# Kernel optimization log

Hardware: AMD Instinct MI355X
Metric: run time of the kernel (lower is better)

Reference implementation:

```python
import jax, jax.numpy as jnp
import numpy as np

N = 16384
C = 128
F = 128

def setup_inputs() -> dict:
    key = jax.random.key(0)
    k1, k2, k3, k4 = jax.random.split(key, 4)
    X = jax.random.normal(k1, (N, C), dtype=jnp.float32)
    adj = jax.random.uniform(k2, (N, N), dtype=jnp.float32)
    W = jax.random.normal(k3, (C, F), dtype=jnp.float32) * 0.05
    b = jax.random.normal(k4, (F,), dtype=jnp.float32) * 0.05
    return {"X": X, "adj": adj, "W": W, "b": b}

def reference(X, adj, W, b):
    # adj_hat = adj + I (self-loops)
    adj_hat = adj + jnp.eye(adj.shape[0], dtype=adj.dtype)
    # D^{-1/2}: inverse of sqrt of the diagonal degree matrix == 1/sqrt(rowsum)
    d_inv_sqrt = 1.0 / jnp.sqrt(jnp.sum(adj_hat, axis=1))  # [N]
    # Symmetric normalization via row/col scaling (same math as D^-1/2 @ A @ D^-1/2)
    adj_norm = adj_hat * d_inv_sqrt[:, None] * d_inv_sqrt[None, :]
    # Feature transform first (N*C*F) then aggregate (N*N*F)
    out = adj_norm @ (X @ W) + b
    return jax.nn.relu(out)
```

## Files before the change

kernel.cpp:

```cpp
#include <hip/hip_runtime.h>
#include <hip/hip_bf16.h>

typedef __attribute__((ext_vector_type(8))) short short8;
typedef __attribute__((ext_vector_type(4))) float f32x4;

#define N_NODES 16384
#define FEAT 128
#define NTILES 256
#define KSPLIT 2
#define NT2 (NTILES / KSPLIT)

__device__ __forceinline__ short f2bf(float x) {
  union { float f; unsigned u; } v;
  v.f = x;
  unsigned r = v.u + 0x7fffu + ((v.u >> 16) & 1u);
  return (short)(r >> 16);
}

__global__ __launch_bounds__(256) void rowsum_kernel(
    const float* __restrict__ adj, float* __restrict__ dinv)
{
  const int row = blockIdx.x;
  const float4* p4 = (const float4*)(adj + (size_t)row * N_NODES);
  float s = 0.f;
  #pragma unroll 4
  for (int i = threadIdx.x; i < N_NODES / 4; i += 256) {
    float4 v = p4[i];
    s += (v.x + v.y) + (v.z + v.w);
  }
  #pragma unroll
  for (int off = 32; off > 0; off >>= 1) s += __shfl_down(s, off, 64);
  __shared__ float part[4];
  if ((threadIdx.x & 63) == 0) part[threadIdx.x >> 6] = s;
  __syncthreads();
  if (threadIdx.x == 0) {
    float tot = (part[0] + part[1]) + (part[2] + part[3]) + 1.0f;
    dinv[row] = rsqrtf(tot);
  }
}

__global__ __launch_bounds__(256) void xw_kernel(
    const float* __restrict__ X, const float* __restrict__ W,
    const float* __restrict__ dinv,
    __hip_bfloat16* __restrict__ Ypack)
{
  __shared__ __align__(16) float Ws[64][128];
  __shared__ __align__(16) float Xs[32][128];
  __shared__ __align__(16) short Ts[128][40];
  const int tid = threadIdx.x;
  const int row0 = blockIdx.x << 5;

  {
    const float4* Xg = (const float4*)(X + ((size_t)row0 << 7));
    float4* Xl = (float4*)&Xs[0][0];
    #pragma unroll
    for (int i = 0; i < 4; ++i) Xl[tid + (i << 8)] = Xg[tid + (i << 8)];
  }
  const int f  = tid & 127;
  const int rr = tid >> 7;
  float acc[16];
  #pragma unroll
  for (int k = 0; k < 16; ++k) acc[k] = 0.f;

  for (int cc = 0; cc < 2; ++cc) {
    __syncthreads();
    {
      const float4* Wg = (const float4*)(W + ((size_t)cc << 13));
      float4* Wl = (float4*)&Ws[0][0];
      #pragma unroll
      for (int i = 0; i < 8; ++i) Wl[tid + (i << 8)] = Wg[tid + (i << 8)];
    }
    __syncthreads();
    for (int c4 = 0; c4 < 16; ++c4) {
      const int cl = c4 << 2;
      const float w0 = Ws[cl + 0][f];
      const float w1 = Ws[cl + 1][f];
      const float w2 = Ws[cl + 2][f];
      const float w3 = Ws[cl + 3][f];
      const int cg = (cc << 6) + cl;
      #pragma unroll
      for (int k = 0; k < 16; ++k) {
        const float4 x = *(const float4*)&Xs[rr + (k << 1)][cg];
        acc[k] += x.x * w0 + x.y * w1 + x.z * w2 + x.w * w3;
      }
    }
  }
  #pragma unroll
  for (int k = 0; k < 16; ++k) {
    const int r = rr + (k << 1);
    const float dv = dinv[row0 + r];
    Ts[f][r] = f2bf(acc[k] * dv);
  }
  __syncthreads();
  {
    const int f2 = tid >> 1;
    const int h  = (tid & 1) << 4;
    const short8 v0 = *(const short8*)&Ts[f2][h];
    const short8 v1 = *(const short8*)&Ts[f2][h + 8];
    short* o = (short*)Ypack;
    *(short8*)(o + (size_t)(row0 + h) * FEAT + (f2 << 3))     = v0;
    *(short8*)(o + (size_t)(row0 + h + 8) * FEAT + (f2 << 3)) = v1;
  }
}

__global__ __launch_bounds__(512, 4) void spmm_kernel(
    const float* __restrict__ A,
    const __hip_bfloat16* __restrict__ Ypack,
    float* __restrict__ pws)
{
  __shared__ __align__(16) short As[2][4096];
  __shared__ __align__(16) short Bs[2][8192];

  const int tid = threadIdx.x;
  const int bid = blockIdx.x;
  const int mt  = bid & 255;
  const int s   = bid >> 8;
  const int row0 = mt << 6;

  const int ar  = tid >> 3;
  const int akg = tid & 7;
  const float* Ag = A + (size_t)(row0 + ar) * N_NODES + (s * NT2 << 6) + (akg << 3);
  const short* Yg = (const short*)Ypack + ((size_t)(s * NT2) << 13) + (tid << 4);

  const int wid  = tid >> 6;
  const int wm   = wid >> 1;
  const int wf   = wid & 1;
  const int lane = tid & 63;
  const int lm   = lane & 15;
  const int lkg  = (lane >> 4);
  const int myrow = (wm << 4) + lm;

  f32x4 acc[4];
  #pragma unroll
  for (int c = 0; c < 4; ++c) acc[c] = (f32x4){0.f, 0.f, 0.f, 0.f};

  float4 a0A, a1A, a0B, a1B;
  short8 y0A, y1A, y0B, y1B;

#define LOADT(T, A0_, A1_, Y0_, Y1_)                                           \
  {                                                                            \
    const float* ap = Ag + ((size_t)(T) << 6);                                 \
    A0_ = *(const float4*)(ap);                                                \
    A1_ = *(const float4*)(ap + 4);                                            \
    const short* yp = Yg + ((size_t)(T) << 13);                                \
    Y0_ = *(const short8*)(yp);                                                \
    Y1_ = *(const short8*)(yp + 8);                                            \
  }

#define STORET(T, P, A0_, A1_, Y0_, Y1_)                                       \
  {                                                                            \
    if (s * NT2 + (T) == mt && (ar >> 3) == akg) {          \
      const int j = ar & 7;                                                    \
      A0_.x += (j == 0) ? 1.f : 0.f;  A0_.y += (j == 1) ? 1.f : 0.f;           \
      A0_.z += (j == 2) ? 1.f : 0.f;  A0_.w += (j == 3) ? 1.f : 0.f;           \
      A1_.x += (j == 4) ? 1.f : 0.f;  A1_.y += (j == 5) ? 1.f : 0.f;           \
      A1_.z += (j == 6) ? 1.f : 0.f;  A1_.w += (j == 7) ? 1.f : 0.f;           \
    }                                                                          \
    short8 av;                                                                 \
    av[0] = f2bf(A0_.x); av[1] = f2bf(A0_.y); av[2] = f2bf(A0_.z);             \
    av[3] = f2bf(A0_.w); av[4] = f2bf(A1_.x); av[5] = f2bf(A1_.y);             \
    av[6] = f2bf(A1_.z); av[7] = f2bf(A1_.w);                                  \
    *(short8*)&As[P][(akg << 9) + (ar << 3)] = av;                             \
    *(short8*)&Bs[P][tid << 4]       = Y0_;                                    \
    *(short8*)&Bs[P][(tid << 4) + 8] = Y1_;                                    \
  }

#define COMP(P)                                                                \
  {                                                                            \
    const short8 af0 = *(const short8*)&As[P][(lkg << 9) + (myrow << 3)];      \
    acc[0] = __builtin_amdgcn_mfma_f32_16x16x32_bf16(af0,                      \
        *(const short8*)&Bs[P][(lkg << 10) + (((wf << 6) + lm) << 3)], acc[0], 0, 0, 0); \
    acc[1] = __builtin_amdgcn_mfma_f32_16x16x32_bf16(af0,                      \
        *(const short8*)&Bs[P][(lkg << 10) + (((wf << 6) + 16 + lm) << 3)], acc[1], 0, 0, 0); \
    acc[2] = __builtin_amdgcn_mfma_f32_16x16x32_bf16(af0,                      \
        *(const short8*)&Bs[P][(lkg << 10) + (((wf << 6) + 32 + lm) << 3)], acc[2], 0, 0, 0); \
    acc[3] = __builtin_amdgcn_mfma_f32_16x16x32_bf16(af0,                      \
        *(const short8*)&Bs[P][(lkg << 10) + (((wf << 6) + 48 + lm) << 3)], acc[3], 0, 0, 0); \
    const short8 af1 = *(const short8*)&As[P][((4 + lkg) << 9) + (myrow << 3)];\
    acc[0] = __builtin_amdgcn_mfma_f32_16x16x32_bf16(af1,                      \
        *(const short8*)&Bs[P][((4 + lkg) << 10) + (((wf << 6) + lm) << 3)], acc[0], 0, 0, 0); \
    acc[1] = __builtin_amdgcn_mfma_f32_16x16x32_bf16(af1,                      \
        *(const short8*)&Bs[P][((4 + lkg) << 10) + (((wf << 6) + 16 + lm) << 3)], acc[1], 0, 0, 0); \
    acc[2] = __builtin_amdgcn_mfma_f32_16x16x32_bf16(af1,                      \
        *(const short8*)&Bs[P][((4 + lkg) << 10) + (((wf << 6) + 32 + lm) << 3)], acc[2], 0, 0, 0); \
    acc[3] = __builtin_amdgcn_mfma_f32_16x16x32_bf16(af1,                      \
        *(const short8*)&Bs[P][((4 + lkg) << 10) + (((wf << 6) + 48 + lm) << 3)], acc[3], 0, 0, 0); \
  }

#define BAR()                                                                  \
  asm volatile("s_waitcnt lgkmcnt(0)" ::: "memory");                           \
  __builtin_amdgcn_s_barrier();

  LOADT(0, a0A, a1A, y0A, y1A)
  LOADT(1, a0B, a1B, y0B, y1B)
  STORET(0, 0, a0A, a1A, y0A, y1A)
  BAR()

  for (int t = 0; t < NT2; t += 2) {
    if (t + 2 < NT2) LOADT(t + 2, a0A, a1A, y0A, y1A)
    __builtin_amdgcn_s_setprio(1);
    COMP(0)
    __builtin_amdgcn_s_setprio(0);
    if (t + 1 < NT2) STORET(t + 1, 1, a0B, a1B, y0B, y1B)
    BAR()
    if (t + 3 < NT2) LOADT(t + 3, a0B, a1B, y0B, y1B)
    __builtin_amdgcn_s_setprio(1);
    COMP(1)
    __builtin_amdgcn_s_setprio(0);
    if (t + 2 < NT2) STORET(t + 2, 0, a0A, a1A, y0A, y1A)
    BAR()
  }

  float* pp = pws + ((size_t)(s * N_NODES + row0)) * FEAT;
  const int lr = (lane >> 4) << 2;
  #pragma unroll
  for (int c = 0; c < 4; ++c) {
    const int col = (wf << 6) + (c << 4) + lm;
    #pragma unroll
    for (int r = 0; r < 4; ++r) {
      pp[(size_t)((wm << 4) + lr + r) * FEAT + col] = acc[c][r];
    }
  }
#undef LOADT
#undef STORET
#undef COMP
#undef BAR
}

__global__ __launch_bounds__(256) void reduce_kernel(
    const float* __restrict__ pws, const float* __restrict__ dinv,
    const float* __restrict__ bias, float* __restrict__ out)
{
  const int idx4 = blockIdx.x * 256 + threadIdx.x;
  const int row  = idx4 >> 5;
  const int f4   = idx4 & 31;
  const float4 p0 = ((const float4*)pws)[idx4];
  const float4 p1 = ((const float4*)pws)[idx4 + (N_NODES * FEAT / 4)];
  const float4 bv = ((const float4*)bias)[f4];
  const float  d  = dinv[row];
  float4 v;
  v.x = d * (p0.x + p1.x) + bv.x;
  v.y = d * (p0.y + p1.y) + bv.y;
  v.z = d * (p0.z + p1.z) + bv.z;
  v.w = d * (p0.w + p1.w) + bv.w;
  v.x = v.x > 0.f ? v.x : 0.f;
  v.y = v.y > 0.f ? v.y : 0.f;
  v.z = v.z > 0.f ? v.z : 0.f;
  v.w = v.w > 0.f ? v.w : 0.f;
  ((float4*)out)[idx4] = v;
}

extern "C" void kernel_launch(void* const* d_in, const int* in_sizes, int n_in,
                              void* d_out, int out_size, void* d_ws, size_t ws_size,
                              hipStream_t stream) {
  const float* X   = (const float*)d_in[0];
  const float* adj = (const float*)d_in[1];
  const float* W   = (const float*)d_in[2];
  const float* b   = (const float*)d_in[3];
  float* out = (float*)d_out;

  float* dinv           = (float*)d_ws;
  __hip_bfloat16* Ypack = (__hip_bfloat16*)((char*)d_ws + (1 << 16));
  float* pws            = (float*)((char*)d_ws + (1 << 16) + (1 << 22));

  rowsum_kernel<<<N_NODES, 256, 0, stream>>>(adj, dinv);
  xw_kernel<<<N_NODES / 32, 256, 0, stream>>>(X, W, dinv, Ypack);
  spmm_kernel<<<NTILES * KSPLIT, 512, 0, stream>>>(adj, Ypack, pws);
  reduce_kernel<<<N_NODES * FEAT / 4 / 256, 256, 0, stream>>>(pws, dinv, b, out);
}
```

Baseline: 409.2 us.

## Load Y tiles directly into LDS with triple buffering and remap block order

```diff
diff --git a/kernel.cpp b/kernel.cpp
--- a/kernel.cpp
+++ b/kernel.cpp
@@ -109,25 +109,26 @@
     float* __restrict__ pws)
 {
   __shared__ __align__(16) short As[2][4096];
-  __shared__ __align__(16) short Bs[2][8192];
+  __shared__ __align__(16) short Bs[3][8192];
 
   const int tid = threadIdx.x;
-  const int bid = blockIdx.x;
-  const int mt  = bid & 255;
-  const int s   = bid >> 8;
+  const int rb  = blockIdx.x;
+  const int lb  = ((rb & 7) << 6) | (rb >> 3);
+  const int mt  = lb & 255;
+  const int s   = lb >> 8;
   const int row0 = mt << 6;
 
   const int ar  = tid >> 3;
   const int akg = tid & 7;
   const float* Ag = A + (size_t)(row0 + ar) * N_NODES + (s * NT2 << 6) + (akg << 3);
-  const short* Yg = (const short*)Ypack + ((size_t)(s * NT2) << 13) + (tid << 4);
+  const short* Yg = (const short*)Ypack + ((size_t)(s * NT2) << 13) + (tid << 3);
 
   const int wid  = tid >> 6;
   const int wm   = wid >> 1;
   const int wf   = wid & 1;
   const int lane = tid & 63;
   const int lm   = lane & 15;
-  const int lkg  = (lane >> 4);
+  const int lkg  = lane >> 4;
   const int myrow = (wm << 4) + lm;
 
   f32x4 acc[4];
@@ -135,19 +136,27 @@
   for (int c = 0; c < 4; ++c) acc[c] = (f32x4){0.f, 0.f, 0.f, 0.f};
 
   float4 a0A, a1A, a0B, a1B;
-  short8 y0A, y1A, y0B, y1B;
-
-#define LOADT(T, A0_, A1_, Y0_, Y1_)                                           \
+
+#define GLDSY(T, P)                                                            \
+  {                                                                            \
+    const short* ys_ = Yg + ((size_t)(T) << 13);                               \
+    __builtin_amdgcn_global_load_lds(                                          \
+        (const __attribute__((address_space(1))) void*)ys_,                    \
+        (__attribute__((address_space(3))) void*)&Bs[P][wid << 9], 16, 0, 0);  \
+    __builtin_amdgcn_global_load_lds(                                          \
+        (const __attribute__((address_space(1))) void*)(ys_ + 4096),           \
+        (__attribute__((address_space(3))) void*)&Bs[P][4096 + (wid << 9)],    \
+        16, 0, 0);                                                             \
+  }
+
+#define LOADA(T, A0_, A1_)                                                     \
   {                                                                            \
     const float* ap = Ag + ((size_t)(T) << 6);                                 \
     A0_ = *(const float4*)(ap);                                                \
     A1_ = *(const float4*)(ap + 4);                                            \
-    const short* yp = Yg + ((size_t)(T) << 13);                                \
-    Y0_ = *(const short8*)(yp);                                                \
-    Y1_ = *(const short8*)(yp + 8);                                            \
-  }
-
-#define STORET(T, P, A0_, A1_, Y0_, Y1_)                                       \
+  }
+
+#define STORA(T, P, A0_, A1_)                                                  \
   {                                                                            \
     if (s * NT2 + (T) == mt && (ar >> 3) == akg) {          \
       const int j = ar & 7;                                                    \
@@ -161,54 +170,62 @@
     av[3] = f2bf(A0_.w); av[4] = f2bf(A1_.x); av[5] = f2bf(A1_.y);             \
     av[6] = f2bf(A1_.z); av[7] = f2bf(A1_.w);                                  \
     *(short8*)&As[P][(akg << 9) + (ar << 3)] = av;                             \
-    *(short8*)&Bs[P][tid << 4]       = Y0_;                                    \
-    *(short8*)&Bs[P][(tid << 4) + 8] = Y1_;                                    \
-  }
-
-#define COMP(P)                                                                \
-  {                                                                            \
-    const short8 af0 = *(const short8*)&As[P][(lkg << 9) + (myrow << 3)];      \
+  }
+
+#define COMP(AP, BP)                                                           \
+  {                                                                            \
+    const short8 af0 = *(const short8*)&As[AP][(lkg << 9) + (myrow << 3)];     \
     acc[0] = __builtin_amdgcn_mfma_f32_16x16x32_bf16(af0,                      \
-        *(const short8*)&Bs[P][(lkg << 10) + (((wf << 6) + lm) << 3)], acc[0], 0, 0, 0); \
+        *(const short8*)&Bs[BP][(lkg << 10) + (((wf << 6) + lm) << 3)], acc[0], 0, 0, 0); \
     acc[1] = __builtin_amdgcn_mfma_f32_16x16x32_bf16(af0,                      \
-        *(const short8*)&Bs[P][(lkg << 10) + (((wf << 6) + 16 + lm) << 3)], acc[1], 0, 0, 0); \
+        *(const short8*)&Bs[BP][(lkg << 10) + (((wf << 6) + 16 + lm) << 3)], acc[1], 0, 0, 0); \
     acc[2] = __builtin_amdgcn_mfma_f32_16x16x32_bf16(af0,                      \
-        *(const short8*)&Bs[P][(lkg << 10) + (((wf << 6) + 32 + lm) << 3)], acc[2], 0, 0, 0); \
+        *(const short8*)&Bs[BP][(lkg << 10) + (((wf << 6) + 32 + lm) << 3)], acc[2], 0, 0, 0); \
     acc[3] = __builtin_amdgcn_mfma_f32_16x16x32_bf16(af0,                      \
-        *(const short8*)&Bs[P][(lkg << 10) + (((wf << 6) + 48 + lm) << 3)], acc[3], 0, 0, 0); \
-    const short8 af1 = *(const short8*)&As[P][((4 + lkg) << 9) + (myrow << 3)];\
+        *(const short8*)&Bs[BP][(lkg << 10) + (((wf << 6) + 48 + lm) << 3)], acc[3], 0, 0, 0); \
+    const short8 af1 = *(const short8*)&As[AP][((4 + lkg) << 9) + (myrow << 3)]; \
     acc[0] = __builtin_amdgcn_mfma_f32_16x16x32_bf16(af1,                      \
-        *(const short8*)&Bs[P][((4 + lkg) << 10) + (((wf << 6) + lm) << 3)], acc[0], 0, 0, 0); \
+        *(const short8*)&Bs[BP][((4 + lkg) << 10) + (((wf << 6) + lm) << 3)], acc[0], 0, 0, 0); \
     acc[1] = __builtin_amdgcn_mfma_f32_16x16x32_bf16(af1,                      \
-        *(const short8*)&Bs[P][((4 + lkg) << 10) + (((wf << 6) + 16 + lm) << 3)], acc[1], 0, 0, 0); \
+        *(const short8*)&Bs[BP][((4 + lkg) << 10) + (((wf << 6) + 16 + lm) << 3)], acc[1], 0, 0, 0); \
     acc[2] = __builtin_amdgcn_mfma_f32_16x16x32_bf16(af1,                      \
-        *(const short8*)&Bs[P][((4 + lkg) << 10) + (((wf << 6) + 32 + lm) << 3)], acc[2], 0, 0, 0); \
+        *(const short8*)&Bs[BP][((4 + lkg) << 10) + (((wf << 6) + 32 + lm) << 3)], acc[2], 0, 0, 0); \
     acc[3] = __builtin_amdgcn_mfma_f32_16x16x32_bf16(af1,                      \
-        *(const short8*)&Bs[P][((4 + lkg) << 10) + (((wf << 6) + 48 + lm) << 3)], acc[3], 0, 0, 0); \
-  }
-
-#define BAR()                                                                  \
-  asm volatile("s_waitcnt lgkmcnt(0)" ::: "memory");                           \
+        *(const short8*)&Bs[BP][((4 + lkg) << 10) + (((wf << 6) + 48 + lm) << 3)], acc[3], 0, 0, 0); \
+  }
+
+  GLDSY(0, 0)
+  LOADA(0, a0A, a1A)
+  GLDSY(1, 1)
+  LOADA(1, a0B, a1B)
+  STORA(0, 0, a0A, a1A)
+  asm volatile("s_waitcnt lgkmcnt(0)" ::: "memory");
   __builtin_amdgcn_s_barrier();
 
-  LOADT(0, a0A, a1A, y0A, y1A)
-  LOADT(1, a0B, a1B, y0B, y1B)
-  STORET(0, 0, a0A, a1A, y0A, y1A)
-  BAR()
-
+  int bp = 0;
   for (int t = 0; t < NT2; t += 2) {
-    if (t + 2 < NT2) LOADT(t + 2, a0A, a1A, y0A, y1A)
+    int bw = bp + 2; if (bw >= 3) bw -= 3;
+    if (t + 2 < NT2) { GLDSY(t + 2, bw) LOADA(t + 2, a0A, a1A) }
     __builtin_amdgcn_s_setprio(1);
-    COMP(0)
+    COMP(0, bp)
     __builtin_amdgcn_s_setprio(0);
-    if (t + 1 < NT2) STORET(t + 1, 1, a0B, a1B, y0B, y1B)
-    BAR()
-    if (t + 3 < NT2) LOADT(t + 3, a0B, a1B, y0B, y1B)
+    if (t + 1 < NT2) STORA(t + 1, 1, a0B, a1B)
+    if (t + 2 < NT2) { asm volatile("s_waitcnt vmcnt(4)" ::: "memory"); }
+    else             { asm volatile("s_waitcnt vmcnt(0)" ::: "memory"); }
+    asm volatile("s_waitcnt lgkmcnt(0)" ::: "memory");
+    __builtin_amdgcn_s_barrier();
+    int bp1 = bp + 1; if (bp1 >= 3) bp1 -= 3;
+    int bw1 = bp1 + 2; if (bw1 >= 3) bw1 -= 3;
+    if (t + 3 < NT2) { GLDSY(t + 3, bw1) LOADA(t + 3, a0B, a1B) }
     __builtin_amdgcn_s_setprio(1);
-    COMP(1)
+    COMP(1, bp1)
     __builtin_amdgcn_s_setprio(0);
-    if (t + 2 < NT2) STORET(t + 2, 0, a0A, a1A, y0A, y1A)
-    BAR()
+    if (t + 2 < NT2) STORA(t + 2, 0, a0A, a1A)
+    if (t + 3 < NT2) { asm volatile("s_waitcnt vmcnt(4)" ::: "memory"); }
+    else             { asm volatile("s_waitcnt vmcnt(0)" ::: "memory"); }
+    asm volatile("s_waitcnt lgkmcnt(0)" ::: "memory");
+    __builtin_amdgcn_s_barrier();
+    bp = bp1 + 1; if (bp >= 3) bp -= 3;
   }
 
   float* pp = pws + ((size_t)(s * N_NODES + row0)) * FEAT;
@@ -221,10 +238,10 @@
       pp[(size_t)((wm << 4) + lr + r) * FEAT + col] = acc[c][r];
     }
   }
-#undef LOADT
-#undef STORET
+#undef GLDSY
+#undef LOADA
+#undef STORA
 #undef COMP
-#undef BAR
 }
 
 __global__ __launch_bounds__(256) void reduce_kernel(
```

Result: no change. 413.4 us (+1.0%).

## Merge rowsum and XW kernels by moving column scaling into SpMM

Applied to the files above, without the earlier changes.

```diff
diff --git a/kernel.cpp b/kernel.cpp
--- a/kernel.cpp
+++ b/kernel.cpp
@@ -17,39 +17,38 @@
   return (short)(r >> 16);
 }
 
-__global__ __launch_bounds__(256) void rowsum_kernel(
-    const float* __restrict__ adj, float* __restrict__ dinv)
-{
-  const int row = blockIdx.x;
-  const float4* p4 = (const float4*)(adj + (size_t)row * N_NODES);
-  float s = 0.f;
-  #pragma unroll 4
-  for (int i = threadIdx.x; i < N_NODES / 4; i += 256) {
-    float4 v = p4[i];
-    s += (v.x + v.y) + (v.z + v.w);
-  }
-  #pragma unroll
-  for (int off = 32; off > 0; off >>= 1) s += __shfl_down(s, off, 64);
-  __shared__ float part[4];
-  if ((threadIdx.x & 63) == 0) part[threadIdx.x >> 6] = s;
-  __syncthreads();
-  if (threadIdx.x == 0) {
-    float tot = (part[0] + part[1]) + (part[2] + part[3]) + 1.0f;
-    dinv[row] = rsqrtf(tot);
-  }
-}
-
-__global__ __launch_bounds__(256) void xw_kernel(
-    const float* __restrict__ X, const float* __restrict__ W,
-    const float* __restrict__ dinv,
-    __hip_bfloat16* __restrict__ Ypack)
+__global__ __launch_bounds__(256) void pre_kernel(
+    const float* __restrict__ adj, const float* __restrict__ X,
+    const float* __restrict__ W, float* __restrict__ dinv,
+    __hip_bfloat16* __restrict__ Upack)
 {
   __shared__ __align__(16) float Ws[64][128];
   __shared__ __align__(16) float Xs[32][128];
   __shared__ __align__(16) short Ts[128][40];
+  __shared__ float part[4];
   const int tid = threadIdx.x;
-  const int row0 = blockIdx.x << 5;
-
+
+  if (blockIdx.x < N_NODES) {
+    const int row = blockIdx.x;
+    const float4* p4 = (const float4*)(adj + (size_t)row * N_NODES);
+    float s = 0.f;
+    #pragma unroll 4
+    for (int i = tid; i < N_NODES / 4; i += 256) {
+      float4 v = p4[i];
+      s += (v.x + v.y) + (v.z + v.w);
+    }
+    #pragma unroll
+    for (int off = 32; off > 0; off >>= 1) s += __shfl_down(s, off, 64);
+    if ((tid & 63) == 0) part[tid >> 6] = s;
+    __syncthreads();
+    if (tid == 0) {
+      float tot = (part[0] + part[1]) + (part[2] + part[3]) + 1.0f;
+      dinv[row] = rsqrtf(tot);
+    }
+    return;
+  }
+
+  const int row0 = (blockIdx.x - N_NODES) << 5;
   {
     const float4* Xg = (const float4*)(X + ((size_t)row0 << 7));
     float4* Xl = (float4*)&Xs[0][0];
@@ -88,8 +87,7 @@
   #pragma unroll
   for (int k = 0; k < 16; ++k) {
     const int r = rr + (k << 1);
-    const float dv = dinv[row0 + r];
-    Ts[f][r] = f2bf(acc[k] * dv);
+    Ts[f][r] = f2bf(acc[k]);
   }
   __syncthreads();
   {
@@ -97,7 +95,7 @@
     const int h  = (tid & 1) << 4;
     const short8 v0 = *(const short8*)&Ts[f2][h];
     const short8 v1 = *(const short8*)&Ts[f2][h + 8];
-    short* o = (short*)Ypack;
+    short* o = (short*)Upack;
     *(short8*)(o + (size_t)(row0 + h) * FEAT + (f2 << 3))     = v0;
     *(short8*)(o + (size_t)(row0 + h + 8) * FEAT + (f2 << 3)) = v1;
   }
@@ -105,7 +103,8 @@
 
 __global__ __launch_bounds__(512, 4) void spmm_kernel(
     const float* __restrict__ A,
-    const __hip_bfloat16* __restrict__ Ypack,
+    const __hip_bfloat16* __restrict__ Upack,
+    const float* __restrict__ dinv,
     float* __restrict__ pws)
 {
   __shared__ __align__(16) short As[2][4096];
@@ -120,34 +119,37 @@
   const int ar  = tid >> 3;
   const int akg = tid & 7;
   const float* Ag = A + (size_t)(row0 + ar) * N_NODES + (s * NT2 << 6) + (akg << 3);
-  const short* Yg = (const short*)Ypack + ((size_t)(s * NT2) << 13) + (tid << 4);
+  const short* Yg = (const short*)Upack + ((size_t)(s * NT2) << 13) + (tid << 4);
 
   const int wid  = tid >> 6;
   const int wm   = wid >> 1;
   const int wf   = wid & 1;
   const int lane = tid & 63;
   const int lm   = lane & 15;
-  const int lkg  = (lane >> 4);
+  const int lkg  = lane >> 4;
   const int myrow = (wm << 4) + lm;
 
   f32x4 acc[4];
   #pragma unroll
   for (int c = 0; c < 4; ++c) acc[c] = (f32x4){0.f, 0.f, 0.f, 0.f};
 
-  float4 a0A, a1A, a0B, a1B;
+  float4 a0A, a1A, a0B, a1B, d0A, d1A, d0B, d1B;
   short8 y0A, y1A, y0B, y1B;
 
-#define LOADT(T, A0_, A1_, Y0_, Y1_)                                           \
+#define LOADT(T, A0_, A1_, D0_, D1_, Y0_, Y1_)                                 \
   {                                                                            \
     const float* ap = Ag + ((size_t)(T) << 6);                                 \
     A0_ = *(const float4*)(ap);                                                \
     A1_ = *(const float4*)(ap + 4);                                            \
+    const float* dp = dinv + ((s * NT2 + (T)) << 6) + (akg << 3);              \
+    D0_ = *(const float4*)(dp);                                                \
+    D1_ = *(const float4*)(dp + 4);                                            \
     const short* yp = Yg + ((size_t)(T) << 13);                                \
     Y0_ = *(const short8*)(yp);                                                \
     Y1_ = *(const short8*)(yp + 8);                                            \
   }
 
-#define STORET(T, P, A0_, A1_, Y0_, Y1_)                                       \
+#define STORET(T, P, A0_, A1_, D0_, D1_, Y0_, Y1_)                             \
   {                                                                            \
     if (s * NT2 + (T) == mt && (ar >> 3) == akg) {          \
       const int j = ar & 7;                                                    \
@@ -156,6 +158,8 @@
       A1_.x += (j == 4) ? 1.f : 0.f;  A1_.y += (j == 5) ? 1.f : 0.f;           \
       A1_.z += (j == 6) ? 1.f : 0.f;  A1_.w += (j == 7) ? 1.f : 0.f;           \
     }                                                                          \
+    A0_.x *= D0_.x; A0_.y *= D0_.y; A0_.z *= D0_.z; A0_.w *= D0_.w;            \
+    A1_.x *= D1_.x; A1_.y *= D1_.y; A1_.z *= D1_.z; A1_.w *= D1_.w;            \
     short8 av;                                                                 \
     av[0] = f2bf(A0_.x); av[1] = f2bf(A0_.y); av[2] = f2bf(A0_.z);             \
     av[3] = f2bf(A0_.w); av[4] = f2bf(A1_.x); av[5] = f2bf(A1_.y);             \
@@ -176,7 +180,7 @@
         *(const short8*)&Bs[P][(lkg << 10) + (((wf << 6) + 32 + lm) << 3)], acc[2], 0, 0, 0); \
     acc[3] = __builtin_amdgcn_mfma_f32_16x16x32_bf16(af0,                      \
         *(const short8*)&Bs[P][(lkg << 10) + (((wf << 6) + 48 + lm) << 3)], acc[3], 0, 0, 0); \
-    const short8 af1 = *(const short8*)&As[P][((4 + lkg) << 9) + (myrow << 3)];\
+    const short8 af1 = *(const short8*)&As[P][((4 + lkg) << 9) + (myrow << 3)]; \
     acc[0] = __builtin_amdgcn_mfma_f32_16x16x32_bf16(af1,                      \
         *(const short8*)&Bs[P][((4 + lkg) << 10) + (((wf << 6) + lm) << 3)], acc[0], 0, 0, 0); \
     acc[1] = __builtin_amdgcn_mfma_f32_16x16x32_bf16(af1,                      \
@@ -191,23 +195,23 @@
   asm volatile("s_waitcnt lgkmcnt(0)" ::: "memory");                           \
   __builtin_amdgcn_s_barrier();
 
-  LOADT(0, a0A, a1A, y0A, y1A)
-  LOADT(1, a0B, a1B, y0B, y1B)
-  STORET(0, 0, a0A, a1A, y0A, y1A)
+  LOADT(0, a0A, a1A, d0A, d1A, y0A, y1A)
+  LOADT(1, a0B, a1B, d0B, d1B, y0B, y1B)
+  STORET(0, 0, a0A, a1A, d0A, d1A, y0A, y1A)
   BAR()
 
   for (int t = 0; t < NT2; t += 2) {
-    if (t + 2 < NT2) LOADT(t + 2, a0A, a1A, y0A, y1A)
+    if (t + 2 < NT2) LOADT(t + 2, a0A, a1A, d0A, d1A, y0A, y1A)
     __builtin_amdgcn_s_setprio(1);
     COMP(0)
     __builtin_amdgcn_s_setprio(0);
-    if (t + 1 < NT2) STORET(t + 1, 1, a0B, a1B, y0B, y1B)
+    if (t + 1 < NT2) STORET(t + 1, 1, a0B, a1B, d0B, d1B, y0B, y1B)
     BAR()
-    if (t + 3 < NT2) LOADT(t + 3, a0B, a1B, y0B, y1B)
+    if (t + 3 < NT2) LOADT(t + 3, a0B, a1B, d0B, d1B, y0B, y1B)
     __builtin_amdgcn_s_setprio(1);
     COMP(1)
     __builtin_amdgcn_s_setprio(0);
-    if (t + 2 < NT2) STORET(t + 2, 0, a0A, a1A, y0A, y1A)
+    if (t + 2 < NT2) STORET(t + 2, 0, a0A, a1A, d0A, d1A, y0A, y1A)
     BAR()
   }
 
@@ -260,11 +264,10 @@
   float* out = (float*)d_out;
 
   float* dinv           = (float*)d_ws;
-  __hip_bfloat16* Ypack = (__hip_bfloat16*)((char*)d_ws + (1 << 16));
+  __hip_bfloat16* Upack = (__hip_bfloat16*)((char*)d_ws + (1 << 16));
   float* pws            = (float*)((char*)d_ws + (1 << 16) + (1 << 22));
 
-  rowsum_kernel<<<N_NODES, 256, 0, stream>>>(adj, dinv);
-  xw_kernel<<<N_NODES / 32, 256, 0, stream>>>(X, W, dinv, Ypack);
-  spmm_kernel<<<NTILES * KSPLIT, 512, 0, stream>>>(adj, Ypack, pws);
+  pre_kernel<<<N_NODES + N_NODES / 32, 256, 0, stream>>>(adj, X, W, dinv, Upack);
+  spmm_kernel<<<NTILES * KSPLIT, 512, 0, stream>>>(adj, Upack, dinv, pws);
   reduce_kernel<<<N_NODES * FEAT / 4 / 256, 256, 0, stream>>>(pws, dinv, b, out);
 }
```

Measured after the change: 413.2 us. Within noise of the previous version (+1.0%).
